# Kernel optimization log

Hardware: AMD Instinct MI355X
Metric: run time of the kernel (lower is better)

## Reference

```python
import jax, jax.numpy as jnp
import numpy as np

B, W = 131072, 32
N_SCEN, SDIM = 19, 16
EMBED_DIM, COMP_DIM = 768, 64
INPUT_DIM = EMBED_DIM + N_SCEN * SDIM  # 1072


def setup_inputs() -> dict:
    key = jax.random.key(0)
    k1, k2, k3, k4, k5, k6 = jax.random.split(key, 6)
    intent_embedding = jax.random.normal(k1, (B, EMBED_DIM), dtype=jnp.float32)
    scenario_ids = jax.random.randint(k2, (B, W), 0, N_SCEN, dtype=jnp.int32)
    # Prefix mask: the torch loop iterates the first int(mask.sum()) slots,
    # so the mask must be a contiguous run of ones.
    lengths = jax.random.randint(k3, (B,), 1, W + 1)
    scenario_mask = (jnp.arange(W)[None, :] < lengths[:, None]).astype(jnp.float32)
    # Parameters (init: normal std=0.01, zero biases)
    scenario_table = 0.01 * jax.random.normal(k4, (N_SCEN, SDIM), dtype=jnp.float32)
    W1 = 0.01 * jax.random.normal(k5, (INPUT_DIM, COMP_DIM), dtype=jnp.float32)
    b1 = jnp.zeros((COMP_DIM,), dtype=jnp.float32)
    W2 = 0.01 * jax.random.normal(k6, (COMP_DIM, 1), dtype=jnp.float32)
    b2 = jnp.zeros((1,), dtype=jnp.float32)
    return {
        "intent_embedding": intent_embedding,
        "scenario_ids": scenario_ids,
        "scenario_mask": scenario_mask,
        "scenario_table": scenario_table,
        "W1": W1, "b1": b1, "W2": W2, "b2": b2,
    }


def reference(intent_embedding, scenario_ids, scenario_mask, scenario_table, W1, b1, W2, b2):
    # Embedding lookup: [B, W, SDIM]
    embeds = scenario_table[scenario_ids]
    masked = embeds * scenario_mask[:, :, None]
    # Vectorized scatter-add into per-scenario bins: [B, N_SCEN, SDIM]
    batch_idx = jnp.arange(scenario_ids.shape[0])[:, None]
    bag3 = jnp.zeros(
        (scenario_ids.shape[0], N_SCEN, SDIM), dtype=embeds.dtype
    ).at[batch_idx, scenario_ids].add(masked)
    counts = scenario_mask.sum(axis=1, keepdims=True)
    bag_vec = bag3.reshape(scenario_ids.shape[0], N_SCEN * SDIM) / jnp.maximum(counts, 1.0)
    combined = jnp.concatenate([intent_embedding, bag_vec], axis=1)  # [B, 1072]
    h = jax.nn.relu(combined @ W1 + b1)  # dropout is identity in eval mode
    return jnp.tanh(h @ W2 + b2)  # [B, 1]
```

## Files before the change

kernel.cpp:

```cpp
#include <hip/hip_runtime.h>
#include <hip/hip_bf16.h>
#include <math.h>

using short8 = __attribute__((ext_vector_type(8))) short;
using f32x4  = __attribute__((ext_vector_type(4))) float;
using fv4    = __attribute__((ext_vector_type(4))) float;

#define EMB 768
#define CD  64
#define NSCEN 19
#define KSTEPS 24
#define NCHUNKS (25 * 4)

__device__ __forceinline__ ushort f2bf(float x) {
    unsigned u = __float_as_uint(x);
    u += 0x7FFFu + ((u >> 16) & 1u);
    return (ushort)(u >> 16);
}

__device__ __forceinline__ uint cvt2(float x, float y) {
    __hip_bfloat162 h = __float22bfloat162_rn(make_float2(x, y));
    union { __hip_bfloat162 h; uint u; } c;
    c.h = h;
    return c.u;
}

__global__ void prep_W1T(const float* __restrict__ table,
                         const float* __restrict__ W1,
                         ushort* __restrict__ W1T) {
    int e = blockIdx.x * 256 + threadIdx.x;
    if (e >= NCHUNKS * 512) return;
    int chunk = e >> 9, r = e & 511;
    int lane = r >> 3, j = r & 7;
    int ks = chunk >> 2, ct = chunk & 3;
    int col = ct * 16 + (lane & 15);
    int k = ks * 32 + ((lane >> 4) << 3) + j;
    float v = 0.f;
    if (k < EMB) {
        v = W1[(size_t)k * CD + col];
    } else {
        int s = k - EMB;
        if (s < NSCEN) {
            for (int d = 0; d < 16; ++d)
                v += table[s * 16 + d] * W1[(size_t)(EMB + s * 16 + d) * CD + col];
        }
    }
    W1T[e] = f2bf(v);
}

__global__ __launch_bounds__(512, 4)
void scorer_mfma(const float* __restrict__ emb,
                 const int* __restrict__ ids,
                 const float* __restrict__ mask,
                 const ushort* __restrict__ W1T,
                 const float* __restrict__ b1,
                 const float* __restrict__ W2,
                 const float* __restrict__ b2,
                 float* __restrict__ out) {
    __shared__ float  bagf[256][21];
    __shared__ ushort bagb[256][32];

    const int t    = threadIdx.x;
    const int w    = t >> 6;
    const int lane = t & 63;
    const int lr   = lane & 15;
    const int lg   = lane >> 4;
    const int row0 = blockIdx.x * 256;

    if (t < 256) {
#pragma unroll
        for (int s = 0; s < NSCEN; ++s) bagf[t][s] = 0.f;
        const int*   idrow = ids  + (size_t)(row0 + t) * 32;
        const float* mrow  = mask + (size_t)(row0 + t) * 32;
        float cnt = 0.f;
#pragma unroll 2
        for (int q = 0; q < 8; ++q) {
            int4   i4 = ((const int4*)idrow)[q];
            float4 m4 = ((const float4*)mrow)[q];
            bagf[t][i4.x] += m4.x; cnt += m4.x;
            bagf[t][i4.y] += m4.y; cnt += m4.y;
            bagf[t][i4.z] += m4.z; cnt += m4.z;
            bagf[t][i4.w] += m4.w; cnt += m4.w;
        }
        float rc = 1.0f / fmaxf(cnt, 1.0f);
#pragma unroll
        for (int s = 0; s < 32; ++s)
            bagb[t][s] = (s < NSCEN) ? f2bf(bagf[t][s] * rc) : (ushort)0;
    }
    __syncthreads();

    const float*  ap = emb + (size_t)(row0 + w * 32 + lr) * EMB + (lg << 3);
    const ushort* wp = W1T + (lane << 3);

    f32x4 acc[2][4];
#pragma unroll
    for (int i = 0; i < 2; ++i)
#pragma unroll
        for (int j = 0; j < 4; ++j) acc[i][j] = (f32x4)0.f;

    fv4    aA[2][2], aB[2][2];
    short8 bbA[4], bbB[4];

#define LOADA(dst, kks) do {                                   \
    const float* _p = ap + (kks) * 32;                         \
    dst[0][0] = *(const fv4*)(_p);                             \
    dst[0][1] = *(const fv4*)(_p + 4);                         \
    dst[1][0] = *(const fv4*)(_p + 16 * EMB);                  \
    dst[1][1] = *(const fv4*)(_p + 16 * EMB + 4);              \
} while (0)

#define LOADB(dst, kks) do {                                   \
    const ushort* _q = wp + ((size_t)(kks) << 11);             \
    dst[0] = *(const short8*)(_q);                             \
    dst[1] = *(const short8*)(_q + 512);                       \
    dst[2] = *(const short8*)(_q + 1024);                      \
    dst[3] = *(const short8*)(_q + 1536);                      \
} while (0)

#define STEP(areg, breg) do {                                              \
    short8 _fa[2];                                                         \
    _Pragma("unroll")                                                      \
    for (int _rt = 0; _rt < 2; ++_rt) {                                    \
        union { uint u[4]; short8 s; } _c;                                 \
        _c.u[0] = cvt2(areg[_rt][0][0], areg[_rt][0][1]);                  \
        _c.u[1] = cvt2(areg[_rt][0][2], areg[_rt][0][3]);                  \
        _c.u[2] = cvt2(areg[_rt][1][0], areg[_rt][1][1]);                  \
        _c.u[3] = cvt2(areg[_rt][1][2], areg[_rt][1][3]);                  \
        _fa[_rt] = _c.s;                                                   \
    }                                                                      \
    _Pragma("unroll")                                                      \
    for (int _rt = 0; _rt < 2; ++_rt) {                                    \
        acc[_rt][0] = __builtin_amdgcn_mfma_f32_16x16x32_bf16(_fa[_rt], breg[0], acc[_rt][0], 0, 0, 0); \
        acc[_rt][1] = __builtin_amdgcn_mfma_f32_16x16x32_bf16(_fa[_rt], breg[1], acc[_rt][1], 0, 0, 0); \
        acc[_rt][2] = __builtin_amdgcn_mfma_f32_16x16x32_bf16(_fa[_rt], breg[2], acc[_rt][2], 0, 0, 0); \
        acc[_rt][3] = __builtin_amdgcn_mfma_f32_16x16x32_bf16(_fa[_rt], breg[3], acc[_rt][3], 0, 0, 0); \
    }                                                                      \
} while (0)

    LOADA(aA, 0);
    LOADB(bbA, 0);
#pragma unroll 1
    for (int ks = 0; ks < KSTEPS; ks += 2) {
        LOADA(aB, ks + 1);
        LOADB(bbB, ks + 1);
        STEP(aA, bbA);
        if (ks + 2 < KSTEPS) {
            LOADA(aA, ks + 2);
            LOADB(bbA, ks + 2);
        } else {
            LOADB(bbA, KSTEPS);
        }
        STEP(aB, bbB);
    }

    {
        short8 ab[2];
        ab[0] = *(const short8*)&bagb[w * 32 + lr][lg << 3];
        ab[1] = *(const short8*)&bagb[w * 32 + 16 + lr][lg << 3];
#pragma unroll
        for (int rt = 0; rt < 2; ++rt) {
            acc[rt][0] = __builtin_amdgcn_mfma_f32_16x16x32_bf16(ab[rt], bbA[0], acc[rt][0], 0, 0, 0);
            acc[rt][1] = __builtin_amdgcn_mfma_f32_16x16x32_bf16(ab[rt], bbA[1], acc[rt][1], 0, 0, 0);
            acc[rt][2] = __builtin_amdgcn_mfma_f32_16x16x32_bf16(ab[rt], bbA[2], acc[rt][2], 0, 0, 0);
            acc[rt][3] = __builtin_amdgcn_mfma_f32_16x16x32_bf16(ab[rt], bbA[3], acc[rt][3], 0, 0, 0);
        }
    }

    float b1v[4], w2v[4];
#pragma unroll
    for (int ct = 0; ct < 4; ++ct) {
        int c = ct * 16 + lr;
        b1v[ct] = b1[c];
        w2v[ct] = W2[c];
    }
    const float b2v = b2[0];
#pragma unroll
    for (int rt = 0; rt < 2; ++rt) {
#pragma unroll
        for (int r = 0; r < 4; ++r) {
            float p = 0.f;
#pragma unroll
            for (int ct = 0; ct < 4; ++ct) {
                float h = acc[rt][ct][r] + b1v[ct];
                p += fmaxf(h, 0.f) * w2v[ct];
            }
            p += __shfl_xor(p, 1);
            p += __shfl_xor(p, 2);
            p += __shfl_xor(p, 4);
            p += __shfl_xor(p, 8);
            if (lr == 0)
                out[row0 + w * 32 + rt * 16 + (lg << 2) + r] = tanhf(p + b2v);
        }
    }
#undef LOADA
#undef LOADB
#undef STEP
}

extern "C" void kernel_launch(void* const* d_in, const int* in_sizes, int n_in,
                              void* d_out, int out_size, void* d_ws, size_t ws_size,
                              hipStream_t stream) {
    const float* emb   = (const float*)d_in[0];
    const int*   ids   = (const int*)d_in[1];
    const float* mask  = (const float*)d_in[2];
    const float* table = (const float*)d_in[3];
    const float* W1    = (const float*)d_in[4];
    const float* b1    = (const float*)d_in[5];
    const float* W2    = (const float*)d_in[6];
    const float* b2    = (const float*)d_in[7];
    float* out  = (float*)d_out;
    ushort* W1T = (ushort*)d_ws;

    prep_W1T<<<200, 256, 0, stream>>>(table, W1, W1T);
    const int nblocks = out_size / 256;
    scorer_mfma<<<nblocks, 512, 0, stream>>>(emb, ids, mask, W1T, b1, W2, b2, out);
}
```

Baseline: 101.5 us.

## Deepen A-prefetch to 4-step groups with nontemporal loads, halve block size

Blocks shrink to 128 rows and 256 threads. The bag build now spreads across all threads, using shared-memory atomics over two halves of each row. The main loop is fully unrolled and prefetches the fp32 activations four K-steps at a time through nontemporal loads, double-buffered, while the bf16 weights go through a 3-deep ring. This aims to keep more HBM loads in flight to hide memory latency on the bandwidth-bound activation stream, at the cost of many more VGPRs and lower occupancy (launch bounds 256,2).

```diff
diff --git a/kernel.cpp b/kernel.cpp
--- a/kernel.cpp
+++ b/kernel.cpp
@@ -11,6 +11,7 @@
 #define NSCEN 19
 #define KSTEPS 24
 #define NCHUNKS (25 * 4)
+#define BM 128
 
 __device__ __forceinline__ ushort f2bf(float x) {
     unsigned u = __float_as_uint(x);
@@ -23,6 +24,10 @@
     union { __hip_bfloat162 h; uint u; } c;
     c.h = h;
     return c.u;
+}
+
+__device__ __forceinline__ fv4 ntl4(const float* p) {
+    return __builtin_nontemporal_load((const fv4*)p);
 }
 
 __global__ void prep_W1T(const float* __restrict__ table,
@@ -48,7 +53,7 @@
     W1T[e] = f2bf(v);
 }
 
-__global__ __launch_bounds__(512, 4)
+__global__ __launch_bounds__(256, 2)
 void scorer_mfma(const float* __restrict__ emb,
                  const int* __restrict__ ids,
                  const float* __restrict__ mask,
@@ -57,35 +62,47 @@
                  const float* __restrict__ W2,
                  const float* __restrict__ b2,
                  float* __restrict__ out) {
-    __shared__ float  bagf[256][21];
-    __shared__ ushort bagb[256][32];
+    __shared__ float  bagf[BM][21];
+    __shared__ ushort bagb[BM][32];
 
     const int t    = threadIdx.x;
     const int w    = t >> 6;
     const int lane = t & 63;
     const int lr   = lane & 15;
     const int lg   = lane >> 4;
-    const int row0 = blockIdx.x * 256;
-
-    if (t < 256) {
-#pragma unroll
-        for (int s = 0; s < NSCEN; ++s) bagf[t][s] = 0.f;
-        const int*   idrow = ids  + (size_t)(row0 + t) * 32;
-        const float* mrow  = mask + (size_t)(row0 + t) * 32;
+    const int row0 = blockIdx.x * BM;
+
+    for (int e = t; e < BM * 21; e += 256) ((float*)bagf)[e] = 0.f;
+    __syncthreads();
+    {
+        const int r = t & (BM - 1), half = t >> 7;
+        const int*   idrow = ids  + (size_t)(row0 + r) * 32 + half * 16;
+        const float* mrow  = mask + (size_t)(row0 + r) * 32 + half * 16;
         float cnt = 0.f;
-#pragma unroll 2
-        for (int q = 0; q < 8; ++q) {
+#pragma unroll
+        for (int q = 0; q < 4; ++q) {
             int4   i4 = ((const int4*)idrow)[q];
             float4 m4 = ((const float4*)mrow)[q];
-            bagf[t][i4.x] += m4.x; cnt += m4.x;
-            bagf[t][i4.y] += m4.y; cnt += m4.y;
-            bagf[t][i4.z] += m4.z; cnt += m4.z;
-            bagf[t][i4.w] += m4.w; cnt += m4.w;
-        }
-        float rc = 1.0f / fmaxf(cnt, 1.0f);
-#pragma unroll
-        for (int s = 0; s < 32; ++s)
-            bagb[t][s] = (s < NSCEN) ? f2bf(bagf[t][s] * rc) : (ushort)0;
+            atomicAdd(&bagf[r][i4.x], m4.x);
+            atomicAdd(&bagf[r][i4.y], m4.y);
+            atomicAdd(&bagf[r][i4.z], m4.z);
+            atomicAdd(&bagf[r][i4.w], m4.w);
+            cnt += m4.x + m4.y + m4.z + m4.w;
+        }
+        atomicAdd(&bagf[r][20], cnt);
+    }
+    __syncthreads();
+    if (t < BM) {
+        float rc = 1.0f / fmaxf(bagf[t][20], 1.0f);
+        union { uint u[16]; short8 s[4]; } cv;
+#pragma unroll
+        for (int p = 0; p < 16; ++p) {
+            float x0 = (2 * p     < NSCEN) ? bagf[t][2 * p] * rc     : 0.f;
+            float x1 = (2 * p + 1 < NSCEN) ? bagf[t][2 * p + 1] * rc : 0.f;
+            cv.u[p] = cvt2(x0, x1);
+        }
+#pragma unroll
+        for (int q = 0; q < 4; ++q) *(short8*)&bagb[t][q * 8] = cv.s[q];
     }
     __syncthreads();
 
@@ -98,15 +115,18 @@
 #pragma unroll
         for (int j = 0; j < 4; ++j) acc[i][j] = (f32x4)0.f;
 
-    fv4    aA[2][2], aB[2][2];
-    short8 bbA[4], bbB[4];
-
-#define LOADA(dst, kks) do {                                   \
-    const float* _p = ap + (kks) * 32;                         \
-    dst[0][0] = *(const fv4*)(_p);                             \
-    dst[0][1] = *(const fv4*)(_p + 4);                         \
-    dst[1][0] = *(const fv4*)(_p + 16 * EMB);                  \
-    dst[1][1] = *(const fv4*)(_p + 16 * EMB + 4);              \
+    fv4    aG[2][4][2][2];
+    short8 bb[3][4];
+
+#define LOADG(dst, gg) do {                                    \
+    _Pragma("unroll")                                          \
+    for (int _s = 0; _s < 4; ++_s) {                           \
+        const float* _p = ap + ((gg) * 4 + _s) * 32;           \
+        dst[_s][0][0] = ntl4(_p);                              \
+        dst[_s][0][1] = ntl4(_p + 4);                          \
+        dst[_s][1][0] = ntl4(_p + 16 * EMB);                   \
+        dst[_s][1][1] = ntl4(_p + 16 * EMB + 4);               \
+    }                                                          \
 } while (0)
 
 #define LOADB(dst, kks) do {                                   \
@@ -137,20 +157,19 @@
     }                                                                      \
 } while (0)
 
-    LOADA(aA, 0);
-    LOADB(bbA, 0);
-#pragma unroll 1
-    for (int ks = 0; ks < KSTEPS; ks += 2) {
-        LOADA(aB, ks + 1);
-        LOADB(bbB, ks + 1);
-        STEP(aA, bbA);
-        if (ks + 2 < KSTEPS) {
-            LOADA(aA, ks + 2);
-            LOADB(bbA, ks + 2);
-        } else {
-            LOADB(bbA, KSTEPS);
-        }
-        STEP(aB, bbB);
+    LOADB(bb[0], 0);
+    LOADB(bb[1], 1);
+    LOADG(aG[0], 0);
+
+#pragma unroll
+    for (int g = 0; g < 6; ++g) {
+        if (g < 5) LOADG(aG[(g + 1) & 1], g + 1);
+#pragma unroll
+        for (int s = 0; s < 4; ++s) {
+            const int ks = g * 4 + s;
+            if (ks + 2 <= KSTEPS) LOADB(bb[(ks + 2) % 3], ks + 2);
+            STEP(aG[g & 1][s], bb[ks % 3]);
+        }
     }
 
     {
@@ -159,10 +178,10 @@
         ab[1] = *(const short8*)&bagb[w * 32 + 16 + lr][lg << 3];
 #pragma unroll
         for (int rt = 0; rt < 2; ++rt) {
-            acc[rt][0] = __builtin_amdgcn_mfma_f32_16x16x32_bf16(ab[rt], bbA[0], acc[rt][0], 0, 0, 0);
-            acc[rt][1] = __builtin_amdgcn_mfma_f32_16x16x32_bf16(ab[rt], bbA[1], acc[rt][1], 0, 0, 0);
-            acc[rt][2] = __builtin_amdgcn_mfma_f32_16x16x32_bf16(ab[rt], bbA[2], acc[rt][2], 0, 0, 0);
-            acc[rt][3] = __builtin_amdgcn_mfma_f32_16x16x32_bf16(ab[rt], bbA[3], acc[rt][3], 0, 0, 0);
+            acc[rt][0] = __builtin_amdgcn_mfma_f32_16x16x32_bf16(ab[rt], bb[0][0], acc[rt][0], 0, 0, 0);
+            acc[rt][1] = __builtin_amdgcn_mfma_f32_16x16x32_bf16(ab[rt], bb[0][1], acc[rt][1], 0, 0, 0);
+            acc[rt][2] = __builtin_amdgcn_mfma_f32_16x16x32_bf16(ab[rt], bb[0][2], acc[rt][2], 0, 0, 0);
+            acc[rt][3] = __builtin_amdgcn_mfma_f32_16x16x32_bf16(ab[rt], bb[0][3], acc[rt][3], 0, 0, 0);
         }
     }
 
@@ -192,7 +211,7 @@
                 out[row0 + w * 32 + rt * 16 + (lg << 2) + r] = tanhf(p + b2v);
         }
     }
-#undef LOADA
+#undef LOADG
 #undef LOADB
 #undef STEP
 }
@@ -212,6 +231,6 @@
     ushort* W1T = (ushort*)d_ws;
 
     prep_W1T<<<200, 256, 0, stream>>>(table, W1, W1T);
-    const int nblocks = out_size / 256;
-    scorer_mfma<<<nblocks, 512, 0, stream>>>(emb, ids, mask, W1T, b1, W2, b2, out);
-}
+    const int nblocks = out_size / BM;
+    scorer_mfma<<<nblocks, 256, 0, stream>>>(emb, ids, mask, W1T, b1, W2, b2, out);
+}
```

Result: slower. 136.5 us (+34.4%).

## Stage W1T weights through double-buffered LDS quarters instead of per-wave global loads

Applied to the files above, without the earlier changes.

Each block now cooperatively loads the bf16 weight matrix in four quarters of six k-steps (plus the bag chunk in the last quarter) into a double-buffered LDS region, with register-staged prefetch of the next quarter. The waves then read B fragments from LDS rather than each wave re-fetching them from global/L2. This cuts redundant global/L2 weight traffic across the 8 waves. In exchange it adds about 57KB of LDS per block, which may limit occupancy against the launch bounds of 4, and inserts block-wide barriers between quarters.

```diff
diff --git a/kernel.cpp b/kernel.cpp
--- a/kernel.cpp
+++ b/kernel.cpp
@@ -11,6 +11,7 @@
 #define NSCEN 19
 #define KSTEPS 24
 #define NCHUNKS (25 * 4)
+#define QB 14336
 
 __device__ __forceinline__ ushort f2bf(float x) {
     unsigned u = __float_as_uint(x);
@@ -57,8 +58,9 @@
                  const float* __restrict__ W2,
                  const float* __restrict__ b2,
                  float* __restrict__ out) {
-    __shared__ float  bagf[256][21];
-    __shared__ ushort bagb[256][32];
+    __shared__ __align__(16) ushort Bq[2][QB];
+    __shared__ __align__(16) ushort bagb[256][32];
+    float* bagf = (float*)&Bq[1][0];
 
     const int t    = threadIdx.x;
     const int w    = t >> 6;
@@ -67,9 +69,27 @@
     const int lg   = lane >> 4;
     const int row0 = blockIdx.x * 256;
 
+    uint4 f0, f1, f2, f3;
+#define ISSUE_FILL(qs) do {                                                  \
+    const uint* _g = (const uint*)((const char*)W1T + (size_t)(qs) * 4096);  \
+    f0 = *(const uint4*)(_g + (t)        * 4);                               \
+    f1 = *(const uint4*)(_g + (t + 512)  * 4);                               \
+    f2 = *(const uint4*)(_g + (t + 1024) * 4);                               \
+    if (t < 256) f3 = *(const uint4*)(_g + (t + 1536) * 4);                  \
+} while (0)
+#define WRITE_FILL(bufi) do {                                                \
+    uint* _l = (uint*)&Bq[bufi][0];                                          \
+    *(uint4*)(_l + (t)        * 4) = f0;                                     \
+    *(uint4*)(_l + (t + 512)  * 4) = f1;                                     \
+    *(uint4*)(_l + (t + 1024) * 4) = f2;                                     \
+    if (t < 256) *(uint4*)(_l + (t + 1536) * 4) = f3;                        \
+} while (0)
+
+    ISSUE_FILL(0);
+
     if (t < 256) {
 #pragma unroll
-        for (int s = 0; s < NSCEN; ++s) bagf[t][s] = 0.f;
+        for (int s = 0; s < NSCEN; ++s) bagf[t * 21 + s] = 0.f;
         const int*   idrow = ids  + (size_t)(row0 + t) * 32;
         const float* mrow  = mask + (size_t)(row0 + t) * 32;
         float cnt = 0.f;
@@ -77,20 +97,22 @@
         for (int q = 0; q < 8; ++q) {
             int4   i4 = ((const int4*)idrow)[q];
             float4 m4 = ((const float4*)mrow)[q];
-            bagf[t][i4.x] += m4.x; cnt += m4.x;
-            bagf[t][i4.y] += m4.y; cnt += m4.y;
-            bagf[t][i4.z] += m4.z; cnt += m4.z;
-            bagf[t][i4.w] += m4.w; cnt += m4.w;
+            bagf[t * 21 + i4.x] += m4.x; cnt += m4.x;
+            bagf[t * 21 + i4.y] += m4.y; cnt += m4.y;
+            bagf[t * 21 + i4.z] += m4.z; cnt += m4.z;
+            bagf[t * 21 + i4.w] += m4.w; cnt += m4.w;
         }
         float rc = 1.0f / fmaxf(cnt, 1.0f);
 #pragma unroll
         for (int s = 0; s < 32; ++s)
-            bagb[t][s] = (s < NSCEN) ? f2bf(bagf[t][s] * rc) : (ushort)0;
-    }
-    __syncthreads();
-
-    const float*  ap = emb + (size_t)(row0 + w * 32 + lr) * EMB + (lg << 3);
-    const ushort* wp = W1T + (lane << 3);
+            bagb[t][s] = (s < NSCEN) ? f2bf(bagf[t * 21 + s] * rc) : (ushort)0;
+    }
+
+    WRITE_FILL(0);
+    ISSUE_FILL(6);
+    __syncthreads();
+
+    const float* ap = emb + (size_t)(row0 + w * 32 + lr) * EMB + (lg << 3);
 
     f32x4 acc[2][4];
 #pragma unroll
@@ -99,7 +121,7 @@
         for (int j = 0; j < 4; ++j) acc[i][j] = (f32x4)0.f;
 
     fv4    aA[2][2], aB[2][2];
-    short8 bbA[4], bbB[4];
+    short8 bqr[4];
 
 #define LOADA(dst, kks) do {                                   \
     const float* _p = ap + (kks) * 32;                         \
@@ -109,60 +131,77 @@
     dst[1][1] = *(const fv4*)(_p + 16 * EMB + 4);              \
 } while (0)
 
-#define LOADB(dst, kks) do {                                   \
-    const ushort* _q = wp + ((size_t)(kks) << 11);             \
-    dst[0] = *(const short8*)(_q);                             \
-    dst[1] = *(const short8*)(_q + 512);                       \
-    dst[2] = *(const short8*)(_q + 1024);                      \
-    dst[3] = *(const short8*)(_q + 1536);                      \
-} while (0)
-
-#define STEP(areg, breg) do {                                              \
-    short8 _fa[2];                                                         \
-    _Pragma("unroll")                                                      \
-    for (int _rt = 0; _rt < 2; ++_rt) {                                    \
-        union { uint u[4]; short8 s; } _c;                                 \
-        _c.u[0] = cvt2(areg[_rt][0][0], areg[_rt][0][1]);                  \
-        _c.u[1] = cvt2(areg[_rt][0][2], areg[_rt][0][3]);                  \
-        _c.u[2] = cvt2(areg[_rt][1][0], areg[_rt][1][1]);                  \
-        _c.u[3] = cvt2(areg[_rt][1][2], areg[_rt][1][3]);                  \
-        _fa[_rt] = _c.s;                                                   \
-    }                                                                      \
-    _Pragma("unroll")                                                      \
-    for (int _rt = 0; _rt < 2; ++_rt) {                                    \
-        acc[_rt][0] = __builtin_amdgcn_mfma_f32_16x16x32_bf16(_fa[_rt], breg[0], acc[_rt][0], 0, 0, 0); \
-        acc[_rt][1] = __builtin_amdgcn_mfma_f32_16x16x32_bf16(_fa[_rt], breg[1], acc[_rt][1], 0, 0, 0); \
-        acc[_rt][2] = __builtin_amdgcn_mfma_f32_16x16x32_bf16(_fa[_rt], breg[2], acc[_rt][2], 0, 0, 0); \
-        acc[_rt][3] = __builtin_amdgcn_mfma_f32_16x16x32_bf16(_fa[_rt], breg[3], acc[_rt][3], 0, 0, 0); \
-    }                                                                      \
+#define LDSB(bufi, ksl) do {                                   \
+    const ushort* _l = &Bq[bufi][(ksl) * 2048 + lane * 8];     \
+    bqr[0] = *(const short8*)(_l);                             \
+    bqr[1] = *(const short8*)(_l + 512);                       \
+    bqr[2] = *(const short8*)(_l + 1024);                      \
+    bqr[3] = *(const short8*)(_l + 1536);                      \
+} while (0)
+
+#define STEP(areg) do {                                                     \
+    short8 _fa[2];                                                          \
+    _Pragma("unroll")                                                       \
+    for (int _rt = 0; _rt < 2; ++_rt) {                                     \
+        union { uint u[4]; short8 s; } _c;                                  \
+        _c.u[0] = cvt2(areg[_rt][0][0], areg[_rt][0][1]);                   \
+        _c.u[1] = cvt2(areg[_rt][0][2], areg[_rt][0][3]);                   \
+        _c.u[2] = cvt2(areg[_rt][1][0], areg[_rt][1][1]);                   \
+        _c.u[3] = cvt2(areg[_rt][1][2], areg[_rt][1][3]);                   \
+        _fa[_rt] = _c.s;                                                    \
+    }                                                                       \
+    _Pragma("unroll")                                                       \
+    for (int _rt = 0; _rt < 2; ++_rt) {                                     \
+        acc[_rt][0] = __builtin_amdgcn_mfma_f32_16x16x32_bf16(_fa[_rt], bqr[0], acc[_rt][0], 0, 0, 0); \
+        acc[_rt][1] = __builtin_amdgcn_mfma_f32_16x16x32_bf16(_fa[_rt], bqr[1], acc[_rt][1], 0, 0, 0); \
+        acc[_rt][2] = __builtin_amdgcn_mfma_f32_16x16x32_bf16(_fa[_rt], bqr[2], acc[_rt][2], 0, 0, 0); \
+        acc[_rt][3] = __builtin_amdgcn_mfma_f32_16x16x32_bf16(_fa[_rt], bqr[3], acc[_rt][3], 0, 0, 0); \
+    }                                                                       \
+} while (0)
+
+#define QUARTER(bufi, qs) do {                                              \
+    _Pragma("unroll")                                                       \
+    for (int _ksl = 0; _ksl < 6; ++_ksl) {                                  \
+        const int _ks = (qs) + _ksl;                                        \
+        LDSB(bufi, _ksl);                                                   \
+        if ((_ks & 1) == 0) {                                               \
+            if (_ks + 1 <= 23) LOADA(aB, _ks + 1);                          \
+            STEP(aA);                                                       \
+        } else {                                                            \
+            if (_ks + 1 <= 23) LOADA(aA, _ks + 1);                          \
+            STEP(aB);                                                       \
+        }                                                                   \
+    }                                                                       \
 } while (0)
 
     LOADA(aA, 0);
-    LOADB(bbA, 0);
-#pragma unroll 1
-    for (int ks = 0; ks < KSTEPS; ks += 2) {
-        LOADA(aB, ks + 1);
-        LOADB(bbB, ks + 1);
-        STEP(aA, bbA);
-        if (ks + 2 < KSTEPS) {
-            LOADA(aA, ks + 2);
-            LOADB(bbA, ks + 2);
-        } else {
-            LOADB(bbA, KSTEPS);
-        }
-        STEP(aB, bbB);
-    }
-
+
+    WRITE_FILL(1);
+    ISSUE_FILL(12);
+    QUARTER(0, 0);
+    __syncthreads();
+
+    WRITE_FILL(0);
+    ISSUE_FILL(18);
+    QUARTER(1, 6);
+    __syncthreads();
+
+    WRITE_FILL(1);
+    QUARTER(0, 12);
+    __syncthreads();
+
+    QUARTER(1, 18);
     {
         short8 ab[2];
         ab[0] = *(const short8*)&bagb[w * 32 + lr][lg << 3];
         ab[1] = *(const short8*)&bagb[w * 32 + 16 + lr][lg << 3];
+        LDSB(1, 6);
 #pragma unroll
         for (int rt = 0; rt < 2; ++rt) {
-            acc[rt][0] = __builtin_amdgcn_mfma_f32_16x16x32_bf16(ab[rt], bbA[0], acc[rt][0], 0, 0, 0);
-            acc[rt][1] = __builtin_amdgcn_mfma_f32_16x16x32_bf16(ab[rt], bbA[1], acc[rt][1], 0, 0, 0);
-            acc[rt][2] = __builtin_amdgcn_mfma_f32_16x16x32_bf16(ab[rt], bbA[2], acc[rt][2], 0, 0, 0);
-            acc[rt][3] = __builtin_amdgcn_mfma_f32_16x16x32_bf16(ab[rt], bbA[3], acc[rt][3], 0, 0, 0);
+            acc[rt][0] = __builtin_amdgcn_mfma_f32_16x16x32_bf16(ab[rt], bqr[0], acc[rt][0], 0, 0, 0);
+            acc[rt][1] = __builtin_amdgcn_mfma_f32_16x16x32_bf16(ab[rt], bqr[1], acc[rt][1], 0, 0, 0);
+            acc[rt][2] = __builtin_amdgcn_mfma_f32_16x16x32_bf16(ab[rt], bqr[2], acc[rt][2], 0, 0, 0);
+            acc[rt][3] = __builtin_amdgcn_mfma_f32_16x16x32_bf16(ab[rt], bqr[3], acc[rt][3], 0, 0, 0);
         }
     }
 
@@ -192,9 +231,12 @@
                 out[row0 + w * 32 + rt * 16 + (lg << 2) + r] = tanhf(p + b2v);
         }
     }
+#undef ISSUE_FILL
+#undef WRITE_FILL
 #undef LOADA
-#undef LOADB
+#undef LDSB
 #undef STEP
+#undef QUARTER
 }
 
 extern "C" void kernel_launch(void* const* d_in, const int* in_sizes, int n_in,
```

After: 95.39 us. -6.1%, faster.
